# Kernel optimization log

Measured on AMD Instinct MI355X. Metric: run time of the kernel, lower is better.

The kernel has to match this reference:

```python
import jax, jax.numpy as jnp
import numpy as np

WORD_VOCAB, WORD_DIM = 50257, 512
CHAR_VOCAB, CHAR_DIM = 262, 128
OUT_DIM = 1024
B, SW, SC = 32, 256, 16
EMB_DIM = WORD_DIM + CHAR_DIM


def setup_inputs() -> dict:
    key = jax.random.key(0)
    ks = jax.random.split(key, 12)
    word_inputs = jax.random.randint(ks[0], (B, SW), 0, WORD_VOCAB)
    char_ids = jax.random.randint(ks[1], (B, SW, SC), 0, CHAR_VOCAB)
    char_lengths = jax.random.randint(ks[2], (B, SW), 1, SC + 1)  # at least 1 char
    word_table = jax.random.normal(ks[3], (WORD_VOCAB, WORD_DIM), jnp.float32) * 0.02
    char_table = jax.random.normal(ks[4], (CHAR_VOCAB, CHAR_DIM), jnp.float32) * 0.02
    # RecursiveCell: gate = Linear(2d -> 3d), project = Linear(2d -> d)
    Wg = jax.random.normal(ks[5], (3 * CHAR_DIM, 2 * CHAR_DIM), jnp.float32) * (1.0 / np.sqrt(2 * CHAR_DIM))
    bg = jnp.zeros((3 * CHAR_DIM,), jnp.float32)
    Wp = jax.random.normal(ks[6], (CHAR_DIM, 2 * CHAR_DIM), jnp.float32) * (1.0 / np.sqrt(2 * CHAR_DIM))
    bp = jnp.zeros((CHAR_DIM,), jnp.float32)
    # final projection Linear(emb_dim -> output_dim)
    W_out = jax.random.normal(ks[7], (OUT_DIM, EMB_DIM), jnp.float32) * (1.0 / np.sqrt(EMB_DIM))
    b_out = jnp.zeros((OUT_DIM,), jnp.float32)
    return {"word_inputs": word_inputs, "char_ids": char_ids, "char_lengths": char_lengths,
            "word_table": word_table, "char_table": char_table,
            "Wg": Wg, "bg": bg, "Wp": Wp, "bp": bp, "W_out": W_out, "b_out": b_out}


def reference(word_inputs, char_ids, char_lengths, word_table, char_table, Wg, bg, Wp, bp, W_out, b_out):
    b, sw = word_inputs.shape
    sc = char_ids.shape[-1]
    d = char_table.shape[-1]
    n = b * sw

    word_emb = word_table[word_inputs]                      # [B, SW, WORD_DIM]

    ids = char_ids.reshape(n, sc)
    lens = char_lengths.reshape(n, 1)
    layer0 = char_table[ids]                                # [N, SC, d]
    pos = jnp.arange(sc)

    def step(layer, length):
        # vectorized RecursiveCell over all adjacent pairs i in [0, SC-2]
        left = layer[:, :-1, :]                             # [N, SC-1, d]
        right = layer[:, 1:, :]                             # [N, SC-1, d]
        flat = jnp.concatenate([left, right], axis=-1)      # [N, SC-1, 2d]
        z = flat @ Wp.T + bp                                # [N, SC-1, d]
        g = jax.nn.softmax((flat @ Wg.T + bg).reshape(n, sc - 1, 3, d), axis=2)
        ret = g[:, :, 0] * left + g[:, :, 1] * right + g[:, :, 2] * z
        new_layer = jnp.pad(ret, ((0, 0), (0, 1), (0, 0)))  # positions >= SC-1 stay zero
        # masked_scatter_: update position i iff i < len - length
        mask = (pos[None, :] < (lens - length))[..., None]  # [N, SC, 1]
        return jnp.where(mask, new_layer, layer), None

    layer, _ = jax.lax.scan(step, layer0, jnp.arange(1, sc))
    char_repr = layer[:, 0, :].reshape(b, sw, d)            # [B, SW, d]

    token_embedding = jnp.concatenate([word_emb, char_repr], axis=-1)
    return token_embedding @ W_out.T + b_out                # [B, SW, OUT_DIM]
```

## Files before the change

kernel.cpp:

```cpp
#include <hip/hip_runtime.h>
#include <hip/hip_bf16.h>

#define NTOK 8192
#define SCC  16
#define CD   128
#define WD   512
#define OD   1024
#define ED   640
#define TW   4
#define LOG2E 1.4426950408889634f

typedef __attribute__((ext_vector_type(8))) short short8;
typedef __attribute__((ext_vector_type(4))) float f32x4;

#if defined(__has_builtin)
#  if __has_builtin(__builtin_amdgcn_exp2f)
#    define EXP2(x) __builtin_amdgcn_exp2f(x)
#  else
#    define EXP2(x) exp2f(x)
#  endif
#else
#  define EXP2(x) exp2f(x)
#endif

__device__ __forceinline__ unsigned short f2bf(float f) {
    union { float f; unsigned u; } v; v.f = f;
    unsigned r = v.u + 0x7FFF + ((v.u >> 16) & 1);
    return (unsigned short)(r >> 16);
}

__device__ __forceinline__ unsigned short f2bf_fast(float f) {
    unsigned r;
    asm("v_cvt_pk_bf16_f32 %0, %1, %2" : "=v"(r) : "v"(f), "v"(f));
    return (unsigned short)r;
}

__global__ void sort_zero(int* s) { if (threadIdx.x < 48) s[threadIdx.x] = 0; }

__global__ void sort_hist(const int* __restrict__ lengths, int* __restrict__ s) {
    const int i = blockIdx.x * 256 + threadIdx.x;
    if (i < NTOK) atomicAdd(&s[lengths[i] - 1], 1);
}

__global__ void sort_prefix(int* s) {
    if (threadIdx.x == 0) {
        int acc = 0;
        for (int b = 15; b >= 0; --b) { s[16 + b] = acc; acc += s[b]; }
    }
}

__global__ __launch_bounds__(256) void sort_scatter_det(
    const int* __restrict__ lengths, int* __restrict__ s)
{
    __shared__ int wsum[4];
    __shared__ int running;
    const int b   = blockIdx.x;
    const int tid = threadIdx.x;
    if (tid == 0) running = s[16 + b];
    __syncthreads();
    for (int c0 = 0; c0 < NTOK; c0 += 256) {
        const int i = c0 + tid;
        const bool f = (lengths[i] - 1 == b);
        const unsigned long long m = __ballot(f);
        const int wv = tid >> 6;
        if ((tid & 63) == 0) wsum[wv] = __popcll(m);
        __syncthreads();
        int excl = 0;
#pragma unroll
        for (int k = 0; k < 4; ++k) if (k < wv) excl += wsum[k];
        const int lanerank = __popcll(m & ((1ull << (tid & 63)) - 1ull));
        if (f) s[48 + running + excl + lanerank] = i;
        const int tot = wsum[0] + wsum[1] + wsum[2] + wsum[3];
        __syncthreads();
        if (tid == 0) running += tot;
        __syncthreads();
    }
}

__global__ __launch_bounds__(256) void pack_weights(
    const float* __restrict__ Wg, const float* __restrict__ Wp,
    uint4* __restrict__ packed)
{
    const int gid  = blockIdx.x * 256 + threadIdx.x;
    const int lane = gid & 63;
    const int kf   = (gid >> 6) & 7;
    const int c    = (gid >> 9) & 3;
    const int w    = (gid >> 11) & 7;
    const int n    = c * 128 + w * 16 + (lane & 15);
    const int k0   = kf * 32 + (lane >> 4) * 8;
    const float sc = (n < 384) ? LOG2E : 1.0f;
    const float* src = (n < 384) ? (Wg + n * 256 + k0) : (Wp + (n - 384) * 256 + k0);
    uint4 o;
    o.x = f2bf(src[0] * sc) | ((unsigned)f2bf(src[1] * sc) << 16);
    o.y = f2bf(src[2] * sc) | ((unsigned)f2bf(src[3] * sc) << 16);
    o.z = f2bf(src[4] * sc) | ((unsigned)f2bf(src[5] * sc) << 16);
    o.w = f2bf(src[6] * sc) | ((unsigned)f2bf(src[7] * sc) << 16);
    packed[gid] = o;
}

__global__ __launch_bounds__(256) void pack_wout(
    const float* __restrict__ W_out, uint4* __restrict__ packed)
{
    const int gid  = blockIdx.x * 256 + threadIdx.x;
    const int lane = gid & 63;
    const int kf   = (gid >> 6) % 20;
    const int nb   = (gid >> 6) / 20;
    const int n    = nb * 16 + (lane & 15);
    const int k0   = kf * 32 + (lane >> 4) * 8;
    const float* src = W_out + (size_t)n * ED + k0;
    uint4 o;
    o.x = f2bf(src[0]) | ((unsigned)f2bf(src[1]) << 16);
    o.y = f2bf(src[2]) | ((unsigned)f2bf(src[3]) << 16);
    o.z = f2bf(src[4]) | ((unsigned)f2bf(src[5]) << 16);
    o.w = f2bf(src[6]) | ((unsigned)f2bf(src[7]) << 16);
    packed[gid] = o;
}

#define LOAD_B(DST, KF)                                                     \
    {                                                                       \
        const uint4* wp_ = Wpacked + (w * 32 + (KF)) * 64 + lane;           \
        union { uint4 u; short8 s; } cv0, cv1, cv2, cv3;                    \
        cv0.u = wp_[0];    DST[0] = cv0.s;                                  \
        cv1.u = wp_[512];  DST[1] = cv1.s;                                  \
        cv2.u = wp_[1024]; DST[2] = cv2.s;                                  \
        cv3.u = wp_[1536]; DST[3] = cv3.s;                                  \
    }

#define LOAD_B_LDS(DST, KFI)                                                \
    {                                                                       \
        const uint4* sp_ = SW + ((w * 4 + (KFI)) * 4) * 64 + lane;          \
        union { uint4 u; short8 s; } d0, d1, d2, d3;                        \
        d0.u = sp_[0];   DST[0] = d0.s;                                     \
        d1.u = sp_[64];  DST[1] = d1.s;                                     \
        d2.u = sp_[128]; DST[2] = d2.s;                                     \
        d3.u = sp_[192]; DST[3] = d3.s;                                     \
    }

#define MFMA_PHASE(BV, KF)                                                  \
    {                                                                       \
        _Pragma("unroll")                                                   \
        for (int m_ = 0; m_ < 4; ++m_) {                                    \
            if (m_ < mfrags) {                                              \
                const int r_ = m_ * 16 + col + (((KF) >= 4) ? 4 : 0);       \
                int ba_ = (r_ << 8) + (((KF) & 3) << 6) + (q << 4);         \
                ba_ ^= (r_ & 15) << 4;                                      \
                const short8 a_ = *reinterpret_cast<const short8*>(Xc + ba_); \
                acc[m_][0] = __builtin_amdgcn_mfma_f32_16x16x32_bf16(a_, BV[0], acc[m_][0], 0, 0, 0); \
                acc[m_][1] = __builtin_amdgcn_mfma_f32_16x16x32_bf16(a_, BV[1], acc[m_][1], 0, 0, 0); \
                acc[m_][2] = __builtin_amdgcn_mfma_f32_16x16x32_bf16(a_, BV[2], acc[m_][2], 0, 0, 0); \
                acc[m_][3] = __builtin_amdgcn_mfma_f32_16x16x32_bf16(a_, BV[3], acc[m_][3], 0, 0, 0); \
            }                                                               \
        }                                                                   \
    }

__global__ __launch_bounds__(512, 2) void scan_mfma(
    const int*   __restrict__ char_ids,
    const int*   __restrict__ char_lengths,
    const float* __restrict__ char_table,
    const float* __restrict__ bg, const float* __restrict__ bp,
    const uint4* __restrict__ Wpacked,
    const int*   __restrict__ order,
    unsigned short* __restrict__ char_repr)
{
    __shared__ __align__(16) unsigned short X[68 * 128];
    __shared__ __align__(16) uint4 SW[8 * 4 * 4 * 64];
    __shared__ int toksh[TW];
    __shared__ int Lsh[TW];

    const int tid  = threadIdx.x;
    const int lane = tid & 63;
    const int w    = tid >> 6;
    const int col  = lane & 15;
    const int q    = lane >> 4;

    if (tid < TW) {
        const int tok = order[blockIdx.x * TW + tid];
        toksh[tid] = tok;
        Lsh[tid]   = char_lengths[tok];
    }

    const int dj = w * 16 + col;
    const float b02 = (bg[dj] - bg[256 + dj]) * LOG2E;
    const float b12 = (bg[128 + dj] - bg[256 + dj]) * LOG2E;
    const float bz  = bp[dj];

    short8 bpin0[4], bpin1[4], bpin6[4], bpin7[4];
    LOAD_B(bpin0, 0);
    LOAD_B(bpin1, 1);
    LOAD_B(bpin6, 6);
    LOAD_B(bpin7, 7);

#pragma unroll
    for (int kfi = 0; kfi < 4; ++kfi)
#pragma unroll
        for (int c = 0; c < 4; ++c)
            SW[((w * 4 + kfi) * 4 + c) * 64 + lane] =
                Wpacked[(w * 32 + c * 8 + (2 + kfi)) * 64 + lane];

    __syncthreads();

    int L[TW];
#pragma unroll
    for (int i = 0; i < TW; ++i) L[i] = Lsh[i];
    const int maxL = max(max(L[0], L[1]), max(L[2], L[3]));

    float stv[4][4];
#pragma unroll
    for (int m = 0; m < 4; ++m) {
        const int p = m * 4 + q;
#pragma unroll
        for (int i = 0; i < 4; ++i) {
            const int id = char_ids[toksh[i] * SCC + p];
            stv[m][i] = char_table[id * CD + dj];
        }
    }

    char* Xc = reinterpret_cast<char*>(X);
#pragma unroll
    for (int m = 0; m < 4; ++m)
#pragma unroll
        for (int i = 0; i < 4; ++i) {
            const int rl = m * 16 + q * 4 + i;
            int bl = (rl << 8) + (dj << 1);
            bl ^= (rl & 15) << 4;
            *reinterpret_cast<unsigned short*>(Xc + bl) = f2bf_fast(stv[m][i]);
        }
    {
        const int r = 64 + (tid >> 7), ku = tid & 63;
    }
    for (int i2 = tid; i2 < 4 * 64; i2 += 512) {
        const int r = 64 + (i2 >> 6), ku = i2 & 63;
        int ba = (r << 8) + (ku << 2);
        ba ^= (r & 15) << 4;
        *reinterpret_cast<unsigned*>(Xc + ba) = 0u;
    }
    __syncthreads();

    for (int len = 1; len < maxL; ++len) {
        const int Amax   = maxL - len;
        const int mfrags = ((4 * Amax + 15) >> 4);

        f32x4 acc[4][4];
#pragma unroll
        for (int m = 0; m < 4; ++m)
#pragma unroll
            for (int c = 0; c < 4; ++c) acc[m][c] = (f32x4){0.f, 0.f, 0.f, 0.f};

        short8 bL[4];
        LOAD_B_LDS(bL, 0);
        MFMA_PHASE(bpin0, 0);
        MFMA_PHASE(bpin1, 1);
        MFMA_PHASE(bL, 2);
        LOAD_B_LDS(bL, 1);
        MFMA_PHASE(bL, 3);
        LOAD_B_LDS(bL, 2);
        MFMA_PHASE(bL, 4);
        LOAD_B_LDS(bL, 3);
        MFMA_PHASE(bL, 5);
        MFMA_PHASE(bpin6, 6);
        MFMA_PHASE(bpin7, 7);

        float shifted[5][4];
#pragma unroll
        for (int m = 0; m < 4; ++m) {
            if (m <= mfrags) {
#pragma unroll
                for (int i = 0; i < 4; ++i)
                    shifted[m][i] = __shfl(stv[m][i], (lane + 16) & 63);
            }
        }
#pragma unroll
        for (int i = 0; i < 4; ++i) shifted[4][i] = 0.f;

#pragma unroll
        for (int m = 0; m < 4; ++m) {
            if (m < mfrags) {
                const int p = m * 4 + q;
#pragma unroll
                for (int i = 0; i < 4; ++i) {
                    const float a0  = acc[m][0][i];
                    const float a1  = acc[m][1][i];
                    const float a2v = acc[m][2][i];
                    const float z   = acc[m][3][i] + bz;
                    const float E0  = EXP2(a0 - a2v + b02);
                    const float E1  = EXP2(a1 - a2v + b12);
                    const float left  = stv[m][i];
                    const float right = (q < 3) ? shifted[m][i] : shifted[m + 1][i];
                    const float inv = __builtin_amdgcn_rcpf(E0 + E1 + 1.0f);
                    const float nv  = (E0 * left + E1 * right + z) * inv;
                    stv[m][i] = (p < L[i] - len) ? nv : stv[m][i];
                }
            }
        }
        __syncthreads();

#pragma unroll
        for (int m = 0; m < 4; ++m) {
            if (m < mfrags) {
#pragma unroll
                for (int i = 0; i < 4; ++i) {
                    const int rl = m * 16 + q * 4 + i;
                    int bl = (rl << 8) + (dj << 1);
                    bl ^= (rl & 15) << 4;
                    *reinterpret_cast<unsigned short*>(Xc + bl) = f2bf_fast(stv[m][i]);
                }
            }
        }
        __syncthreads();
    }

    if (q == 0) {
#pragma unroll
        for (int i = 0; i < 4; ++i)
            char_repr[toksh[i] * CD + dj] = f2bf_fast(stv[0][i]);
    }
}

#define TPB2 32

__global__ __launch_bounds__(512) void out_mfma(
    const int*   __restrict__ word_inputs,
    const float* __restrict__ word_table,
    const unsigned short* __restrict__ char_repr,
    const uint4* __restrict__ pwout,
    const float* __restrict__ b_out,
    float*       __restrict__ out)
{
    __shared__ __align__(16) unsigned short E[TPB2 * ED];

    const int tg   = blockIdx.x * TPB2;
    const int tid  = threadIdx.x;
    const int lane = tid & 63;
    const int w    = tid >> 6;
    const int col  = lane & 15;
    const int q    = lane >> 4;

    for (int i = tid; i < TPB2 * 256; i += 512) {
        const int rt = i >> 8, kp = i & 255;
        const float2 v = *reinterpret_cast<const float2*>(
            word_table + (size_t)word_inputs[tg + rt] * WD + 2 * kp);
        const unsigned u = f2bf(v.x) | ((unsigned)f2bf(v.y) << 16);
        int baddr = rt * 1280 + kp * 4;
        baddr ^= (rt & 7) << 4;
        *reinterpret_cast<unsigned*>(reinterpret_cast<char*>(E) + baddr) = u;
    }
    for (int i = tid; i < TPB2 * 64; i += 512) {
        const int rt = i >> 6, kp = i & 63;
        const unsigned u = *reinterpret_cast<const unsigned*>(
            char_repr + (tg + rt) * CD + 2 * kp);
        int baddr = rt * 1280 + 1024 + kp * 4;
        baddr ^= (rt & 7) << 4;
        *reinterpret_cast<unsigned*>(reinterpret_cast<char*>(E) + baddr) = u;
    }
    __syncthreads();

    f32x4 acc[2][8];
#pragma unroll
    for (int mm = 0; mm < 2; ++mm)
#pragma unroll
        for (int nf = 0; nf < 8; ++nf) acc[mm][nf] = (f32x4){0.f, 0.f, 0.f, 0.f};

#pragma unroll 4
    for (int kf = 0; kf < 20; ++kf) {
        short8 a[2];
#pragma unroll
        for (int mm = 0; mm < 2; ++mm) {
            const int row = mm * 16 + col;
            int ba = row * 1280 + kf * 64 + q * 16;
            ba ^= (row & 7) << 4;
            a[mm] = *reinterpret_cast<const short8*>(
                reinterpret_cast<const char*>(E) + ba);
        }
#pragma unroll
        for (int nf = 0; nf < 8; ++nf) {
            const int nb = w * 8 + nf;
            union { uint4 u; short8 s; } cv;
            cv.u = pwout[(nb * 20 + kf) * 64 + lane];
            acc[0][nf] = __builtin_amdgcn_mfma_f32_16x16x32_bf16(a[0], cv.s, acc[0][nf], 0, 0, 0);
            acc[1][nf] = __builtin_amdgcn_mfma_f32_16x16x32_bf16(a[1], cv.s, acc[1][nf], 0, 0, 0);
        }
    }

#pragma unroll
    for (int nf = 0; nf < 8; ++nf) {
        const int j = (w * 8 + nf) * 16 + col;
        const float bias = b_out[j];
#pragma unroll
        for (int mm = 0; mm < 2; ++mm)
#pragma unroll
            for (int i = 0; i < 4; ++i) {
                out[(size_t)(tg + mm * 16 + q * 4 + i) * OD + j] = acc[mm][nf][i] + bias;
            }
    }
}


extern "C" void kernel_launch(void* const* d_in, const int* in_sizes, int n_in,
                              void* d_out, int out_size, void* d_ws, size_t ws_size,
                              hipStream_t stream)
{
    const int*   word_inputs  = (const int*)  d_in[0];
    const int*   char_ids     = (const int*)  d_in[1];
    const int*   char_lengths = (const int*)  d_in[2];
    const float* word_table   = (const float*)d_in[3];
    const float* char_table   = (const float*)d_in[4];
    const float* Wg           = (const float*)d_in[5];
    const float* bg           = (const float*)d_in[6];
    const float* Wp           = (const float*)d_in[7];
    const float* bp           = (const float*)d_in[8];
    const float* W_out        = (const float*)d_in[9];
    const float* b_out        = (const float*)d_in[10];

    float* out = (float*)d_out;
    char* ws = (char*)d_ws;
    unsigned short* char_repr = (unsigned short*)ws;
    uint4* Wpacked = (uint4*)(ws + 2 * 1024 * 1024);
    int*   sortbuf = (int*)(ws + 2 * 1024 * 1024 + 256 * 1024);
    const int* order = sortbuf + 48;
    uint4* pwout = (uint4*)(ws + 2 * 1024 * 1024 + 256 * 1024 + 64 * 1024);

    pack_weights<<<64, 256, 0, stream>>>(Wg, Wp, Wpacked);
    pack_wout<<<320, 256, 0, stream>>>(W_out, pwout);
    sort_zero<<<1, 64, 0, stream>>>(sortbuf);
    sort_hist<<<NTOK / 256, 256, 0, stream>>>(char_lengths, sortbuf);
    sort_prefix<<<1, 64, 0, stream>>>(sortbuf);
    sort_scatter_det<<<16, 256, 0, stream>>>(char_lengths, sortbuf);

    scan_mfma<<<NTOK / TW, 512, 0, stream>>>(char_ids, char_lengths, char_table,
                                             bg, bp, Wpacked, order, char_repr);
    out_mfma<<<NTOK / TPB2, 512, 0, stream>>>(word_inputs, word_table, char_repr,
                                              pwout, b_out, out);
}
```

Baseline: 264.8 us.

## Stream scan weights from global per k-fragment to raise occupancy

```diff
diff --git a/kernel.cpp b/kernel.cpp
--- a/kernel.cpp
+++ b/kernel.cpp
@@ -116,44 +116,7 @@
     packed[gid] = o;
 }
 
-#define LOAD_B(DST, KF)                                                     \
-    {                                                                       \
-        const uint4* wp_ = Wpacked + (w * 32 + (KF)) * 64 + lane;           \
-        union { uint4 u; short8 s; } cv0, cv1, cv2, cv3;                    \
-        cv0.u = wp_[0];    DST[0] = cv0.s;                                  \
-        cv1.u = wp_[512];  DST[1] = cv1.s;                                  \
-        cv2.u = wp_[1024]; DST[2] = cv2.s;                                  \
-        cv3.u = wp_[1536]; DST[3] = cv3.s;                                  \
-    }
-
-#define LOAD_B_LDS(DST, KFI)                                                \
-    {                                                                       \
-        const uint4* sp_ = SW + ((w * 4 + (KFI)) * 4) * 64 + lane;          \
-        union { uint4 u; short8 s; } d0, d1, d2, d3;                        \
-        d0.u = sp_[0];   DST[0] = d0.s;                                     \
-        d1.u = sp_[64];  DST[1] = d1.s;                                     \
-        d2.u = sp_[128]; DST[2] = d2.s;                                     \
-        d3.u = sp_[192]; DST[3] = d3.s;                                     \
-    }
-
-#define MFMA_PHASE(BV, KF)                                                  \
-    {                                                                       \
-        _Pragma("unroll")                                                   \
-        for (int m_ = 0; m_ < 4; ++m_) {                                    \
-            if (m_ < mfrags) {                                              \
-                const int r_ = m_ * 16 + col + (((KF) >= 4) ? 4 : 0);       \
-                int ba_ = (r_ << 8) + (((KF) & 3) << 6) + (q << 4);         \
-                ba_ ^= (r_ & 15) << 4;                                      \
-                const short8 a_ = *reinterpret_cast<const short8*>(Xc + ba_); \
-                acc[m_][0] = __builtin_amdgcn_mfma_f32_16x16x32_bf16(a_, BV[0], acc[m_][0], 0, 0, 0); \
-                acc[m_][1] = __builtin_amdgcn_mfma_f32_16x16x32_bf16(a_, BV[1], acc[m_][1], 0, 0, 0); \
-                acc[m_][2] = __builtin_amdgcn_mfma_f32_16x16x32_bf16(a_, BV[2], acc[m_][2], 0, 0, 0); \
-                acc[m_][3] = __builtin_amdgcn_mfma_f32_16x16x32_bf16(a_, BV[3], acc[m_][3], 0, 0, 0); \
-            }                                                               \
-        }                                                                   \
-    }
-
-__global__ __launch_bounds__(512, 2) void scan_mfma(
+__global__ __launch_bounds__(512, 4) void scan_mfma(
     const int*   __restrict__ char_ids,
     const int*   __restrict__ char_lengths,
     const float* __restrict__ char_table,
@@ -163,7 +126,6 @@
     unsigned short* __restrict__ char_repr)
 {
     __shared__ __align__(16) unsigned short X[68 * 128];
-    __shared__ __align__(16) uint4 SW[8 * 4 * 4 * 64];
     __shared__ int toksh[TW];
     __shared__ int Lsh[TW];
 
@@ -184,19 +146,6 @@
     const float b12 = (bg[128 + dj] - bg[256 + dj]) * LOG2E;
     const float bz  = bp[dj];
 
-    short8 bpin0[4], bpin1[4], bpin6[4], bpin7[4];
-    LOAD_B(bpin0, 0);
-    LOAD_B(bpin1, 1);
-    LOAD_B(bpin6, 6);
-    LOAD_B(bpin7, 7);
-
-#pragma unroll
-    for (int kfi = 0; kfi < 4; ++kfi)
-#pragma unroll
-        for (int c = 0; c < 4; ++c)
-            SW[((w * 4 + kfi) * 4 + c) * 64 + lane] =
-                Wpacked[(w * 32 + c * 8 + (2 + kfi)) * 64 + lane];
-
     __syncthreads();
 
     int L[TW];
@@ -225,9 +174,6 @@
             bl ^= (rl & 15) << 4;
             *reinterpret_cast<unsigned short*>(Xc + bl) = f2bf_fast(stv[m][i]);
         }
-    {
-        const int r = 64 + (tid >> 7), ku = tid & 63;
-    }
     for (int i2 = tid; i2 < 4 * 64; i2 += 512) {
         const int r = 64 + (i2 >> 6), ku = i2 & 63;
         int ba = (r << 8) + (ku << 2);
@@ -246,31 +192,33 @@
 #pragma unroll
             for (int c = 0; c < 4; ++c) acc[m][c] = (f32x4){0.f, 0.f, 0.f, 0.f};
 
-        short8 bL[4];
-        LOAD_B_LDS(bL, 0);
-        MFMA_PHASE(bpin0, 0);
-        MFMA_PHASE(bpin1, 1);
-        MFMA_PHASE(bL, 2);
-        LOAD_B_LDS(bL, 1);
-        MFMA_PHASE(bL, 3);
-        LOAD_B_LDS(bL, 2);
-        MFMA_PHASE(bL, 4);
-        LOAD_B_LDS(bL, 3);
-        MFMA_PHASE(bL, 5);
-        MFMA_PHASE(bpin6, 6);
-        MFMA_PHASE(bpin7, 7);
-
-        float shifted[5][4];
-#pragma unroll
-        for (int m = 0; m < 4; ++m) {
-            if (m <= mfrags) {
-#pragma unroll
-                for (int i = 0; i < 4; ++i)
-                    shifted[m][i] = __shfl(stv[m][i], (lane + 16) & 63);
-            }
-        }
-#pragma unroll
-        for (int i = 0; i < 4; ++i) shifted[4][i] = 0.f;
+#pragma unroll 1
+        for (int kf = 0; kf < 8; ++kf) {
+            short8 b[4];
+            {
+                const uint4* wp_ = Wpacked + (w * 32 + kf) * 64 + lane;
+                union { uint4 u; short8 s; } cv0, cv1, cv2, cv3;
+                cv0.u = wp_[0];    b[0] = cv0.s;
+                cv1.u = wp_[512];  b[1] = cv1.s;
+                cv2.u = wp_[1024]; b[2] = cv2.s;
+                cv3.u = wp_[1536]; b[3] = cv3.s;
+            }
+            const int rofs = (kf >= 4) ? 4 : 0;
+            const int kofs = (kf & 3) << 6;
+#pragma unroll
+            for (int m = 0; m < 4; ++m) {
+                if (m < mfrags) {
+                    const int r_ = m * 16 + col + rofs;
+                    int ba_ = (r_ << 8) + kofs + (q << 4);
+                    ba_ ^= (r_ & 15) << 4;
+                    const short8 a_ = *reinterpret_cast<const short8*>(Xc + ba_);
+                    acc[m][0] = __builtin_amdgcn_mfma_f32_16x16x32_bf16(a_, b[0], acc[m][0], 0, 0, 0);
+                    acc[m][1] = __builtin_amdgcn_mfma_f32_16x16x32_bf16(a_, b[1], acc[m][1], 0, 0, 0);
+                    acc[m][2] = __builtin_amdgcn_mfma_f32_16x16x32_bf16(a_, b[2], acc[m][2], 0, 0, 0);
+                    acc[m][3] = __builtin_amdgcn_mfma_f32_16x16x32_bf16(a_, b[3], acc[m][3], 0, 0, 0);
+                }
+            }
+        }
 
 #pragma unroll
         for (int m = 0; m < 4; ++m) {
@@ -284,8 +232,10 @@
                     const float z   = acc[m][3][i] + bz;
                     const float E0  = EXP2(a0 - a2v + b02);
                     const float E1  = EXP2(a1 - a2v + b12);
+                    const float shf  = __shfl(stv[m][i], (lane + 16) & 63);
+                    const float shfn = (m < 3) ? __shfl(stv[m + 1][i], (lane + 16) & 63) : 0.f;
                     const float left  = stv[m][i];
-                    const float right = (q < 3) ? shifted[m][i] : shifted[m + 1][i];
+                    const float right = (q < 3) ? shf : shfn;
                     const float inv = __builtin_amdgcn_rcpf(E0 + E1 + 1.0f);
                     const float nv  = (E0 * left + E1 * right + z) * inv;
                     stv[m][i] = (p < L[i] - len) ? nv : stv[m][i];
```

Result: no change. 268.3 us (+1.3%).
